# Optimization experiments

Hardware: AMD Instinct MI355X
Metric: run time of the kernel (lower is better)

The kernel has to match this reference:

```python
import jax, jax.numpy as jnp
from jax import lax
import numpy as np

P = 4        # pool_size
NH = 8       # nhead
EPS = 1e-5


def _maxpool(x):
    return lax.reduce_window(x, -jnp.inf, lax.max, (1, 1, P, P), (1, 1, P, P), 'VALID')


def _ln_c(x, g, b):
    # LayerNorm over channel dim of NCHW (torch applies it on NHWC last dim)
    m = x.mean(1, keepdims=True)
    v = x.var(1, keepdims=True)
    return g[None, :, None, None] * (x - m) / jnp.sqrt(v + EPS) + b[None, :, None, None]


def _dwbn(x, w, g, b, rm, rv):
    # depthwise 3x3 conv (groups=C, no bias) + BatchNorm2d (inference, running stats)
    C = x.shape[1]
    y = lax.conv_general_dilated(x, w, (1, 1), ((1, 1), (1, 1)),
                                 dimension_numbers=('NCHW', 'OIHW', 'NCHW'),
                                 feature_group_count=C)
    sc = g / jnp.sqrt(rv + EPS)
    return sc[None, :, None, None] * (y - rm[None, :, None, None]) + b[None, :, None, None]


def _heads(x):
    # n (nhead d) h w -> n (h w) nhead d
    B, C, H, W = x.shape
    return x.reshape(B, NH, C // NH, H * W).transpose(0, 3, 1, 2)


def _fuse(x, m, merge_w, mlp_w1, mlp_w2, ln2_g, ln2_b):
    # merge linear -> reshape to pooled map -> bilinear upsample x4 -> concat -> MLP -> LN -> residual
    B, C, H, W = x.shape
    m = jnp.einsum('nlh d -> nlhd', m) if False else m  # no-op, keep m as [B,L,NH,dim]
    m = m.reshape(B, -1, C) @ merge_w.T                  # [B, L, C]
    m = m.reshape(B, H // P, W // P, C).transpose(0, 3, 1, 2)
    m = jax.image.resize(m, (B, C, H, W), method='bilinear')  # align_corners=False convention
    z = jnp.concatenate([x, m], axis=1).transpose(0, 2, 3, 1)  # NHWC, 2C
    z = jax.nn.relu(z @ mlp_w1.T) @ mlp_w2.T                   # [B,H,W,C]
    mu = z.mean(-1, keepdims=True)
    var = z.var(-1, keepdims=True)
    z = ln2_g * (z - mu) / jnp.sqrt(var + EPS) + ln2_b
    return x + z.transpose(0, 3, 1, 2)


def setup_inputs() -> dict:
    key = jax.random.key(0)
    ks = jax.random.split(key, 20)
    B, C, H, W = 4, 256, 128, 128
    s = 0.05
    return {
        'x1': jax.random.normal(ks[0], (B, C, H, W), jnp.float32),
        'x2': jax.random.normal(ks[1], (B, C, H, W), jnp.float32),
        'qk_w': jax.random.normal(ks[2], (C, 1, 3, 3), jnp.float32) * s,
        'qk_g': 1.0 + 0.1 * jax.random.normal(ks[3], (C,), jnp.float32),
        'qk_b': 0.1 * jax.random.normal(ks[4], (C,), jnp.float32),
        'qk_m': 0.1 * jax.random.normal(ks[5], (C,), jnp.float32),
        'qk_v': jax.random.uniform(ks[6], (C,), jnp.float32, 0.5, 1.5),
        'v_w': jax.random.normal(ks[7], (C, 1, 3, 3), jnp.float32) * s,
        'v_g': 1.0 + 0.1 * jax.random.normal(ks[8], (C,), jnp.float32),
        'v_b': 0.1 * jax.random.normal(ks[9], (C,), jnp.float32),
        'v_m': 0.1 * jax.random.normal(ks[10], (C,), jnp.float32),
        'v_v': jax.random.uniform(ks[11], (C,), jnp.float32, 0.5, 1.5),
        'ln1_g': 1.0 + 0.1 * jax.random.normal(ks[12], (C,), jnp.float32),
        'ln1_b': 0.1 * jax.random.normal(ks[13], (C,), jnp.float32),
        'ln2_g': 1.0 + 0.1 * jax.random.normal(ks[14], (C,), jnp.float32),
        'ln2_b': 0.1 * jax.random.normal(ks[15], (C,), jnp.float32),
        'merge_w': jax.random.normal(ks[16], (C, C), jnp.float32) * s,
        'mlp_w1': jax.random.normal(ks[17], (2 * C, 2 * C), jnp.float32) * s,
        'mlp_w2': jax.random.normal(ks[18], (C, 2 * C), jnp.float32) * s,
    }


def reference(x1, x2, qk_w, qk_g, qk_b, qk_m, qk_v, v_w, v_g, v_b, v_m, v_v,
              ln1_g, ln1_b, ln2_g, ln2_b, merge_w, mlp_w1, mlp_w2):
    # pooled + normalized features (norm1 shared across q/k/v branches)
    p1 = _ln_c(_maxpool(x1), ln1_g, ln1_b)
    p2 = _ln_c(_maxpool(x2), ln1_g, ln1_b)
    query = _heads(_dwbn(p1, qk_w, qk_g, qk_b, qk_m, qk_v))  # [B,L,NH,d]
    key = _heads(_dwbn(p2, qk_w, qk_g, qk_b, qk_m, qk_v))    # [B,S,NH,d]
    v1h = _heads(_dwbn(p1, v_w, v_g, v_b, v_m, v_v))
    v2h = _heads(_dwbn(p2, v_w, v_g, v_b, v_m, v_v))
    QK = jnp.einsum('nlhd,nshd->nlsh', query, key).astype(jnp.float32)
    t = 1.0 / np.sqrt(query.shape[-1]).astype(np.float32)
    S1 = jax.nn.softmax(t * QK, axis=2)   # softmax over s (keys)
    S2 = jax.nn.softmax(t * QK, axis=3)   # softmax over head dim (as in source)
    m1 = jnp.einsum('nlsh,nshd->nlhd', S1, v2h)
    m2 = jnp.einsum('nlsh,nlhd->nshd', S2, v1h)
    out1 = _fuse(x1, m1, merge_w, mlp_w1, mlp_w2, ln2_g, ln2_b)
    out2 = _fuse(x2, m2, merge_w, mlp_w1, mlp_w2, ln2_g, ln2_b)
    return (out1, out2)
```

## Files before the change

### kernel.cpp

```cpp
#include <hip/hip_runtime.h>
#include <hip/hip_bf16.h>

#define NB 4
#define NC 256
#define NH_ 8
#define LPOOL 1024
constexpr float EPSV = 1e-5f;

typedef unsigned short ushort_t;
typedef __attribute__((ext_vector_type(8))) short bf16x8;
typedef __attribute__((ext_vector_type(4))) float f32x4;

#define OFF_P   0u
#define OFF_V2T 1048576u
#define OFF_Q   2097152u
#define OFF_K   3145728u
#define OFF_V1  4194304u
#define OFF_V2  5242880u
#define OFF_M1  6291456u
#define OFF_M2  7340032u
#define OFF_MG  8388608u
#define OFF_A   9437184u
#define OFF_W1B 26214400u
#define OFF_W2B 26345472u
#define OFF_HID 42991616u

__device__ __forceinline__ float bf16_to_f(unsigned short u) {
    union { unsigned int ui; float f; } t; t.ui = ((unsigned int)u) << 16; return t.f;
}
__device__ __forceinline__ unsigned short f_to_bf16(float f) {
    union { float f; unsigned int u; } t; t.f = f;
    unsigned int u = t.u;
    u += 0x7fffu + ((u >> 16) & 1u);
    return (unsigned short)(u >> 16);
}

__global__ __launch_bounds__(256) void pool_kernel(const float* __restrict__ x1,
                                                   const float* __restrict__ x2,
                                                   float* __restrict__ pooled) {
    int idx = blockIdx.x * 256 + threadIdx.x;
    int j = idx & 31, i = (idx >> 5) & 31, c = (idx >> 10) & 255, n = (idx >> 18) & 3, br = idx >> 20;
    const float* xp = br ? x2 : x1;
    const float* base = xp + (((size_t)(n * 256 + c) * 128 + i * 4) * 128 + j * 4);
    float m = -3.4e38f;
#pragma unroll
    for (int r = 0; r < 4; ++r) {
        float4 v = *(const float4*)(base + r * 128);
        m = fmaxf(m, fmaxf(fmaxf(v.x, v.y), fmaxf(v.z, v.w)));
    }
    pooled[(size_t)br * 1048576 + (size_t)(n * 256 + c) * 1024 + i * 32 + j] = m;
}

__global__ __launch_bounds__(256) void lnc_kernel(float* __restrict__ p,
                                                  const float* __restrict__ g,
                                                  const float* __restrict__ b) {
    int bid = blockIdx.x;
    int l = bid & 1023, n = (bid >> 10) & 3, br = bid >> 12;
    int c = threadIdx.x;
    size_t idx = (size_t)br * 1048576 + (size_t)(n * 256 + c) * 1024 + l;
    float v = p[idx];
    __shared__ float red[256];
    red[c] = v; __syncthreads();
    for (int off = 128; off > 0; off >>= 1) { if (c < off) red[c] += red[c + off]; __syncthreads(); }
    float mean = red[0] / 256.f;
    __syncthreads();
    float d = v - mean;
    red[c] = d * d; __syncthreads();
    for (int off = 128; off > 0; off >>= 1) { if (c < off) red[c] += red[c + off]; __syncthreads(); }
    float var = red[0] / 256.f;
    float rstd = rsqrtf(var + EPSV);
    p[idx] = (v - mean) * rstd * g[c] + b[c];
}

__global__ __launch_bounds__(256) void dwbn_kernel(const float* __restrict__ p,
    const float* __restrict__ qkw, const float* __restrict__ qkg, const float* __restrict__ qkb,
    const float* __restrict__ qkm, const float* __restrict__ qkv,
    const float* __restrict__ vw, const float* __restrict__ vg, const float* __restrict__ vb,
    const float* __restrict__ vm, const float* __restrict__ vv,
    float* __restrict__ qkvbuf) {
    int which = blockIdx.y;
    int flat = blockIdx.x * 256 + threadIdx.x;
    int l = flat & 1023, c = (flat >> 10) & 255, n = flat >> 18;
    int br = which & 1;
    const float* w  = (which < 2) ? qkw : vw;
    const float* g  = (which < 2) ? qkg : vg;
    const float* bb = (which < 2) ? qkb : vb;
    const float* rm = (which < 2) ? qkm : vm;
    const float* rv = (which < 2) ? qkv : vv;
    int i = l >> 5, j = l & 31;
    const float* pin = p + (size_t)br * 1048576 + (size_t)(n * 256 + c) * 1024;
    float acc = 0.f;
#pragma unroll
    for (int ky = -1; ky <= 1; ++ky) {
        int yy = i + ky;
        if ((unsigned)yy < 32u) {
#pragma unroll
            for (int kx = -1; kx <= 1; ++kx) {
                int xx = j + kx;
                if ((unsigned)xx < 32u)
                    acc += pin[yy * 32 + xx] * w[c * 9 + (ky + 1) * 3 + (kx + 1)];
            }
        }
    }
    float sc = g[c] * rsqrtf(rv[c] + EPSV);
    qkvbuf[(size_t)which * 1048576 + (size_t)(n * 1024 + l) * 256 + c] = sc * (acc - rm[c]) + bb[c];
}

__global__ __launch_bounds__(256) void cvt_kernel(const float* __restrict__ in,
                                                  ushort_t* __restrict__ out, int n) {
    int i = blockIdx.x * 256 + threadIdx.x;
    if (i < n) out[i] = f_to_bf16(in[i]);
}

__global__ __launch_bounds__(256) void v2t_kernel(const float* __restrict__ v,
                                                  ushort_t* __restrict__ vt) {
    int bid = blockIdx.x;
    int sb = bid & 31, cb = (bid >> 5) & 7, n = bid >> 8;
    int tid = threadIdx.x;
    __shared__ float t[32][33];
    int ci = tid & 31, sg = tid >> 5;
#pragma unroll
    for (int p = 0; p < 4; ++p) {
        int s = sb * 32 + p * 8 + sg;
        t[p * 8 + sg][ci] = v[(size_t)(n * 1024 + s) * 256 + cb * 32 + ci];
    }
    __syncthreads();
    int si = tid & 31, cg = tid >> 5;
#pragma unroll
    for (int p = 0; p < 4; ++p) {
        int c = cb * 32 + p * 8 + cg;
        vt[(size_t)(n * 256 + c) * 1024 + sb * 32 + si] = f_to_bf16(t[si][p * 8 + cg]);
    }
}

__global__ __launch_bounds__(256) void qk_mfma(const ushort_t* __restrict__ qb,
                                               const ushort_t* __restrict__ kb,
                                               float* __restrict__ scores) {
    int lt = blockIdx.x, st = blockIdx.y;
    int nh = blockIdx.z; int n = nh >> 3, h = nh & 7;
    int l0 = lt * 128, s0 = st * 128;
    __shared__ ushort_t Qs[128 * 32];
    __shared__ ushort_t Ks[128 * 32];
    int tid = threadIdx.x, lane = tid & 63, wv = tid >> 6;
    int wm = wv >> 1, wn = wv & 1;
    int ml = lane & 15, quad = lane >> 4;
#pragma unroll
    for (int c = 0; c < 2; ++c) {
        int g = c * 256 + tid;
        int row = g >> 2, seg = g & 3;
        const ushort_t* ga = qb + (size_t)(n * 1024 + l0 + row) * 256 + h * 32 + seg * 8;
        __builtin_amdgcn_global_load_lds((const __attribute__((address_space(1))) void*)ga,
                                         (__attribute__((address_space(3))) void*)&Qs[row * 32 + seg * 8], 16, 0, 0);
        const ushort_t* gk = kb + (size_t)(n * 1024 + s0 + row) * 256 + h * 32 + seg * 8;
        __builtin_amdgcn_global_load_lds((const __attribute__((address_space(1))) void*)gk,
                                         (__attribute__((address_space(3))) void*)&Ks[row * 32 + seg * 8], 16, 0, 0);
    }
    __syncthreads();
    f32x4 acc[4][4];
#pragma unroll
    for (int i = 0; i < 4; ++i)
#pragma unroll
        for (int j = 0; j < 4; ++j) acc[i][j] = (f32x4)(0.f);
    bf16x8 af[4], bfr[4];
#pragma unroll
    for (int mt = 0; mt < 4; ++mt)
        af[mt] = *(const bf16x8*)&Qs[(wm * 64 + mt * 16 + ml) * 32 + quad * 8];
#pragma unroll
    for (int nt = 0; nt < 4; ++nt)
        bfr[nt] = *(const bf16x8*)&Ks[(wn * 64 + nt * 16 + ml) * 32 + quad * 8];
#pragma unroll
    for (int mt = 0; mt < 4; ++mt)
#pragma unroll
        for (int nt = 0; nt < 4; ++nt)
            acc[mt][nt] = __builtin_amdgcn_mfma_f32_16x16x32_bf16(af[mt], bfr[nt], acc[mt][nt], 0, 0, 0);
    const float tsc = 0.17677669529663687f;
    float* sb = scores + (size_t)nh * 1024 * 1024;
#pragma unroll
    for (int mt = 0; mt < 4; ++mt)
#pragma unroll
        for (int nt = 0; nt < 4; ++nt) {
            int col = s0 + wn * 64 + nt * 16 + ml;
#pragma unroll
            for (int r = 0; r < 4; ++r) {
                int row = l0 + wm * 64 + mt * 16 + quad * 4 + r;
                sb[(size_t)row * 1024 + col] = tsc * acc[mt][nt][r];
            }
        }
}

__global__ __launch_bounds__(256) void m1_kernel(const float* __restrict__ scores,
                                                 const ushort_t* __restrict__ v2t,
                                                 float* __restrict__ m1out) {
    int lt = blockIdx.x, h = blockIdx.y, n = blockIdx.z;
    int tid = threadIdx.x, lane = tid & 63, wv = tid >> 6;
    int ml = lane & 15, quad = lane >> 4;
    int l0 = lt * 64 + wv * 16;
    const float* arow = scores + (size_t)((n * 8 + h) * 1024 + l0 + ml) * 1024 + quad * 8;
    const ushort_t* vb = v2t + (size_t)(n * 256 + h * 32) * 1024;
    const ushort_t* vrow0 = vb + (size_t)ml * 1024 + quad * 8;
    const ushort_t* vrow1 = vb + (size_t)(ml + 16) * 1024 + quad * 8;
    f32x4 acc0 = (f32x4)(0.f), acc1 = (f32x4)(0.f);
    float rsum = 0.f;
#pragma unroll 4
    for (int s0 = 0; s0 < 1024; s0 += 32) {
        float4 xa = *(const float4*)(arow + s0);
        float4 xb = *(const float4*)(arow + s0 + 4);
        float e0 = __expf(xa.x), e1 = __expf(xa.y), e2 = __expf(xa.z), e3 = __expf(xa.w);
        float e4 = __expf(xb.x), e5 = __expf(xb.y), e6 = __expf(xb.z), e7 = __expf(xb.w);
        rsum += ((e0 + e1) + (e2 + e3)) + ((e4 + e5) + (e6 + e7));
        bf16x8 af;
        af[0] = (short)f_to_bf16(e0); af[1] = (short)f_to_bf16(e1);
        af[2] = (short)f_to_bf16(e2); af[3] = (short)f_to_bf16(e3);
        af[4] = (short)f_to_bf16(e4); af[5] = (short)f_to_bf16(e5);
        af[6] = (short)f_to_bf16(e6); af[7] = (short)f_to_bf16(e7);
        bf16x8 b0 = *(const bf16x8*)(vrow0 + s0);
        bf16x8 b1 = *(const bf16x8*)(vrow1 + s0);
        acc0 = __builtin_amdgcn_mfma_f32_16x16x32_bf16(af, b0, acc0, 0, 0, 0);
        acc1 = __builtin_amdgcn_mfma_f32_16x16x32_bf16(af, b1, acc1, 0, 0, 0);
    }
    rsum += __shfl_xor(rsum, 16);
    rsum += __shfl_xor(rsum, 32);
#pragma unroll
    for (int r = 0; r < 4; ++r) {
        int row = quad * 4 + r;
        float inv = 1.f / __shfl(rsum, row);
        size_t ob = (size_t)(n * 1024 + l0 + row) * 256 + h * 32;
        m1out[ob + ml] = acc0[r] * inv;
        m1out[ob + 16 + ml] = acc1[r] * inv;
    }
}

__global__ __launch_bounds__(256) void m2_kernel(const float* __restrict__ scores,
                                                 const float* __restrict__ v1,
                                                 float* __restrict__ m2out) {
    int st = blockIdx.x;
    int lc = blockIdx.y;
    int n  = blockIdx.z;
    int s0 = st * 32, tid = threadIdx.x;
    __shared__ float wls[8][8][32];
    float acc[32];
#pragma unroll
    for (int i = 0; i < 32; ++i) acc[i] = 0.f;
    int lA = tid >> 5, siA = tid & 31;
    int hB = tid >> 5;
    const float* sbase = scores + (size_t)n * 8 * 1024 * 1024;
    int lend = lc * 128 + 128;
    for (int lb = lc * 128; lb < lend; lb += 8) {
        int l = lb + lA;
        float e[8];
        float mx = -3.4e38f;
#pragma unroll
        for (int h = 0; h < 8; ++h) {
            e[h] = sbase[((size_t)h * 1024 + l) * 1024 + s0 + siA];
            mx = fmaxf(mx, e[h]);
        }
        float sum = 0.f;
#pragma unroll
        for (int h = 0; h < 8; ++h) { e[h] = expf(e[h] - mx); sum += e[h]; }
        float inv = 1.f / sum;
#pragma unroll
        for (int h = 0; h < 8; ++h) wls[lA][h][siA] = e[h] * inv;
        __syncthreads();
#pragma unroll
        for (int ls = 0; ls < 8; ++ls) {
            float v1v = v1[(size_t)(n * 1024 + lb + ls) * 256 + tid];
#pragma unroll
            for (int s4 = 0; s4 < 8; ++s4) {
                float4 w4 = *(const float4*)&wls[ls][hB][s4 * 4];
                acc[s4 * 4]     += w4.x * v1v;
                acc[s4 * 4 + 1] += w4.y * v1v;
                acc[s4 * 4 + 2] += w4.z * v1v;
                acc[s4 * 4 + 3] += w4.w * v1v;
            }
        }
        __syncthreads();
    }
#pragma unroll
    for (int ss = 0; ss < 32; ++ss)
        atomicAdd(&m2out[(size_t)(n * 1024 + s0 + ss) * 256 + tid], acc[ss]);
}

__global__ __launch_bounds__(256) void merge_kernel(const float* __restrict__ m,
                                                    const float* __restrict__ mw,
                                                    float* __restrict__ merged) {
    int bid = blockIdx.x;
    int n = bid >> 7, lt = bid & 127;
    int l0 = lt * 8, tid = threadIdx.x;
    __shared__ float ms[8][260];
#pragma unroll
    for (int r = 0; r < 8; ++r) ms[r][tid] = m[(size_t)(n * 1024 + l0 + r) * 256 + tid];
    __syncthreads();
    float acc[8];
#pragma unroll
    for (int r = 0; r < 8; ++r) acc[r] = 0.f;
    const float4* wrow = (const float4*)(mw + (size_t)tid * 256);
    for (int c4 = 0; c4 < 64; ++c4) {
        float4 w4 = wrow[c4];
#pragma unroll
        for (int r = 0; r < 8; ++r) {
            float4 m4 = *(const float4*)&ms[r][c4 * 4];
            acc[r] += w4.x * m4.x + w4.y * m4.y + w4.z * m4.z + w4.w * m4.w;
        }
    }
#pragma unroll
    for (int r = 0; r < 8; ++r)
        merged[(size_t)(n * 1024 + l0 + r) * 256 + tid] = acc[r];
}

__global__ __launch_bounds__(256) void zbuild_kernel(const float* __restrict__ x,
                                                     const float* __restrict__ merged,
                                                     ushort_t* __restrict__ z) {
    int pix0 = blockIdx.x * 32;
    int n = pix0 >> 14, y = (pix0 >> 7) & 127, x0 = pix0 & 127;
    int tid = threadIdx.x;
    int ci = tid >> 5, xi = tid & 31;
    __shared__ float xs[256][33];
    for (int cc = 0; cc < 32; ++cc) {
        int c = cc * 8 + ci;
        xs[c][xi] = x[((size_t)(n * 256 + c) * 128 + y) * 128 + x0 + xi];
    }
    __syncthreads();
    float iy = y * 0.25f - 0.375f;
    int y0i = (int)floorf(iy);
    float fy = iy - (float)y0i;
    int y0c = max(y0i, 0), y1c = min(y0i + 1, 31);
    const float* mb = merged + (size_t)n * 1024 * 256;
    for (int xj = 0; xj < 32; ++xj) {
        size_t zb = (size_t)(pix0 + xj) * 512;
        z[zb + tid] = f_to_bf16(xs[tid][xj]);
        int xx = x0 + xj;
        float ix = xx * 0.25f - 0.375f;
        int x0i = (int)floorf(ix);
        float fx = ix - (float)x0i;
        int x0cc = max(x0i, 0), x1cc = min(x0i + 1, 31);
        float v00 = mb[(size_t)(y0c * 32 + x0cc) * 256 + tid];
        float v01 = mb[(size_t)(y0c * 32 + x1cc) * 256 + tid];
        float v10 = mb[(size_t)(y1c * 32 + x0cc) * 256 + tid];
        float v11 = mb[(size_t)(y1c * 32 + x1cc) * 256 + tid];
        float v = (1.f - fy) * ((1.f - fx) * v00 + fx * v01) + fy * ((1.f - fx) * v10 + fx * v11);
        z[zb + 256 + tid] = f_to_bf16(v);
    }
}

__global__ __launch_bounds__(256) void mfma_gemm(const ushort_t* __restrict__ A,
                                                 const ushort_t* __restrict__ B,
                                                 float* __restrict__ Of,
                                                 ushort_t* __restrict__ Oh,
                                                 int N, int relu) {
    const int K = 512;
    int m0 = blockIdx.x * 128, n0 = blockIdx.y * 128;
    int tid = threadIdx.x;
    __shared__ ushort_t Al[128 * 32];
    __shared__ ushort_t Bl[128 * 32];
    int lane = tid & 63;
    int wv = tid >> 6;
    int wm = wv >> 1, wn = wv & 1;
    int ml = lane & 15, quad = lane >> 4;
    f32x4 acc[4][4];
#pragma unroll
    for (int i = 0; i < 4; ++i)
#pragma unroll
        for (int j = 0; j < 4; ++j) acc[i][j] = (f32x4)(0.f);

    for (int k0 = 0; k0 < K; k0 += 32) {
#pragma unroll
        for (int c = 0; c < 2; ++c) {
            int g = c * 256 + tid;
            int row = g >> 2, seg = g & 3;
            const ushort_t* ga = A + (size_t)(m0 + row) * K + k0 + seg * 8;
            __builtin_amdgcn_global_load_lds((const __attribute__((address_space(1))) void*)ga,
                                             (__attribute__((address_space(3))) void*)&Al[g * 8], 16, 0, 0);
            const ushort_t* gb = B + (size_t)(n0 + row) * K + k0 + seg * 8;
            __builtin_amdgcn_global_load_lds((const __attribute__((address_space(1))) void*)gb,
                                             (__attribute__((address_space(3))) void*)&Bl[g * 8], 16, 0, 0);
        }
        __syncthreads();
        bf16x8 af[4], bfr[4];
#pragma unroll
        for (int mt = 0; mt < 4; ++mt)
            af[mt] = *(const bf16x8*)&Al[(wm * 64 + mt * 16 + ml) * 32 + quad * 8];
#pragma unroll
        for (int nt = 0; nt < 4; ++nt)
            bfr[nt] = *(const bf16x8*)&Bl[(wn * 64 + nt * 16 + ml) * 32 + quad * 8];
#pragma unroll
        for (int mt = 0; mt < 4; ++mt)
#pragma unroll
            for (int nt = 0; nt < 4; ++nt)
                acc[mt][nt] = __builtin_amdgcn_mfma_f32_16x16x32_bf16(af[mt], bfr[nt], acc[mt][nt], 0, 0, 0);
        __syncthreads();
    }
#pragma unroll
    for (int mt = 0; mt < 4; ++mt) {
#pragma unroll
        for (int nt = 0; nt < 4; ++nt) {
            int col = n0 + wn * 64 + nt * 16 + ml;
#pragma unroll
            for (int r = 0; r < 4; ++r) {
                int row = m0 + wm * 64 + mt * 16 + quad * 4 + r;
                float v = acc[mt][nt][r];
                if (relu) v = fmaxf(v, 0.f);
                if (Oh) Oh[(size_t)row * N + col] = f_to_bf16(v);
                else    Of[(size_t)row * N + col] = v;
            }
        }
    }
}

__global__ __launch_bounds__(256) void final_kernel(const float* __restrict__ o,
                                                    const float* __restrict__ xin,
                                                    const float* __restrict__ g,
                                                    const float* __restrict__ b,
                                                    float* __restrict__ outp) {
    int xg = blockIdx.x, y = blockIdx.y, n = blockIdx.z;
    int x0 = xg * 32;
    int pix0 = (n * 128 + y) * 128 + x0;
    int tid = threadIdx.x;
    __shared__ float zf[32][257];
    for (int j = 0; j < 32; ++j) zf[j][tid] = o[(size_t)(pix0 + j) * 256 + tid];
    __syncthreads();
    __shared__ float rs[32][9], rq[32][9];
    __shared__ float muA[32], rsA[32];
    int p = tid >> 3, q = tid & 7;
    float s = 0.f, sq = 0.f;
    for (int c = q * 32; c < q * 32 + 32; ++c) { float v = zf[p][c]; s += v; sq += v * v; }
    rs[p][q] = s; rq[p][q] = sq; __syncthreads();
    if (q == 0) {
        float S = 0.f, Q = 0.f;
#pragma unroll
        for (int t = 0; t < 8; ++t) { S += rs[p][t]; Q += rq[p][t]; }
        float mu = S / 256.f;
        float var = Q / 256.f - mu * mu;
        muA[p] = mu; rsA[p] = rsqrtf(var + EPSV);
    }
    __syncthreads();
    int cg = tid >> 5, xi = tid & 31;
    for (int cc = 0; cc < 32; ++cc) {
        int c = cc * 8 + cg;
        float v = (zf[xi][c] - muA[xi]) * rsA[xi] * g[c] + b[c];
        size_t gi = ((size_t)(n * 256 + c) * 128 + y) * 128 + x0 + xi;
        outp[gi] = xin[gi] + v;
    }
}

extern "C" void kernel_launch(void* const* d_in, const int* in_sizes, int n_in,
                              void* d_out, int out_size, void* d_ws, size_t ws_size,
                              hipStream_t stream) {
    (void)in_sizes; (void)n_in; (void)out_size; (void)ws_size;
    const float* x1     = (const float*)d_in[0];
    const float* x2     = (const float*)d_in[1];
    const float* qk_w   = (const float*)d_in[2];
    const float* qk_g   = (const float*)d_in[3];
    const float* qk_b   = (const float*)d_in[4];
    const float* qk_m   = (const float*)d_in[5];
    const float* qk_v   = (const float*)d_in[6];
    const float* v_w    = (const float*)d_in[7];
    const float* v_g    = (const float*)d_in[8];
    const float* v_b    = (const float*)d_in[9];
    const float* v_m    = (const float*)d_in[10];
    const float* v_v    = (const float*)d_in[11];
    const float* ln1_g  = (const float*)d_in[12];
    const float* ln1_b  = (const float*)d_in[13];
    const float* ln2_g  = (const float*)d_in[14];
    const float* ln2_b  = (const float*)d_in[15];
    const float* merge_w = (const float*)d_in[16];
    const float* mlp_w1 = (const float*)d_in[17];
    const float* mlp_w2 = (const float*)d_in[18];

    float* ws      = (float*)d_ws;
    float* pooled  = ws + OFF_P;
    float* qkvbuf  = ws + OFF_Q;
    float* v1buf   = ws + OFF_V1;
    float* v2buf   = ws + OFF_V2;
    float* m1buf   = ws + OFF_M1;
    float* m2buf   = ws + OFF_M2;
    float* mgbuf   = ws + OFF_MG;
    float* regA    = ws + OFF_A;
    ushort_t* qkb16 = (ushort_t*)(ws + OFF_P);
    ushort_t* v2tb = (ushort_t*)(ws + OFF_V2T);
    ushort_t* zb16 = (ushort_t*)(ws + OFF_A);
    ushort_t* w1b  = (ushort_t*)(ws + OFF_W1B);
    ushort_t* w2b  = (ushort_t*)(ws + OFF_W2B);
    ushort_t* hid  = (ushort_t*)(ws + OFF_HID);
    float* outp    = (float*)d_out;

    hipMemsetAsync(m2buf, 0, 1048576 * sizeof(float), stream);

    pool_kernel<<<8192, 256, 0, stream>>>(x1, x2, pooled);
    lnc_kernel<<<8192, 256, 0, stream>>>(pooled, ln1_g, ln1_b);
    dwbn_kernel<<<dim3(4096, 4), 256, 0, stream>>>(pooled,
        qk_w, qk_g, qk_b, qk_m, qk_v, v_w, v_g, v_b, v_m, v_v, qkvbuf);
    cvt_kernel<<<8192, 256, 0, stream>>>(qkvbuf, qkb16, 2097152);
    v2t_kernel<<<1024, 256, 0, stream>>>(v2buf, v2tb);
    qk_mfma<<<dim3(8, 8, 32), 256, 0, stream>>>(qkb16, qkb16 + 1048576, regA);
    m1_kernel<<<dim3(16, 8, 4), 256, 0, stream>>>(regA, v2tb, m1buf);
    m2_kernel<<<dim3(32, 8, 4), 256, 0, stream>>>(regA, v1buf, m2buf);

    cvt_kernel<<<1024, 256, 0, stream>>>(mlp_w1, w1b, 262144);
    cvt_kernel<<<512, 256, 0, stream>>>(mlp_w2, w2b, 131072);

    for (int br = 0; br < 2; ++br) {
        const float* xin = br ? x2 : x1;
        const float* mm  = br ? m2buf : m1buf;
        merge_kernel<<<512, 256, 0, stream>>>(mm, merge_w, mgbuf);
        zbuild_kernel<<<2048, 256, 0, stream>>>(xin, mgbuf, zb16);
        mfma_gemm<<<dim3(512, 4), 256, 0, stream>>>(zb16, w1b, nullptr, hid, 512, 1);
        mfma_gemm<<<dim3(512, 2), 256, 0, stream>>>(hid, w2b, regA, nullptr, 256, 0);
        final_kernel<<<dim3(4, 128, 4), 256, 0, stream>>>(regA, xin, ln2_g, ln2_b,
                                                          outp + (size_t)br * 16777216);
    }
}
```

Measured before the change: 816.1 us.

## Fuse MLP GEMMs with LayerNorm/residual and store attention scores in bf16

Replaces the two separate MLP GEMM launches and the final LayerNorm/residual kernel with a single fused kernel per branch. Each block computes a 64-row tile of the hidden layer, keeps it in swizzled LDS, and then runs the second GEMM, the LayerNorm and the residual add before writing NCHW output. This removes the global round trips for the hidden activations and the pre-norm output. Attention scores are also written and read as bf16 instead of fp32, which halves score traffic but lowers softmax input precision. The fused kernel reads A/B operands straight from global memory without LDS staging and uses a large LDS footprint, which may limit occupancy.

```diff
diff --git a/kernel.cpp b/kernel.cpp
--- a/kernel.cpp
+++ b/kernel.cpp
@@ -23,7 +23,6 @@
 #define OFF_A   9437184u
 #define OFF_W1B 26214400u
 #define OFF_W2B 26345472u
-#define OFF_HID 42991616u
 
 __device__ __forceinline__ float bf16_to_f(unsigned short u) {
     union { unsigned int ui; float f; } t; t.ui = ((unsigned int)u) << 16; return t.f;
@@ -135,7 +134,7 @@
 
 __global__ __launch_bounds__(256) void qk_mfma(const ushort_t* __restrict__ qb,
                                                const ushort_t* __restrict__ kb,
-                                               float* __restrict__ scores) {
+                                               ushort_t* __restrict__ scores) {
     int lt = blockIdx.x, st = blockIdx.y;
     int nh = blockIdx.z; int n = nh >> 3, h = nh & 7;
     int l0 = lt * 128, s0 = st * 128;
@@ -174,7 +173,7 @@
         for (int nt = 0; nt < 4; ++nt)
             acc[mt][nt] = __builtin_amdgcn_mfma_f32_16x16x32_bf16(af[mt], bfr[nt], acc[mt][nt], 0, 0, 0);
     const float tsc = 0.17677669529663687f;
-    float* sb = scores + (size_t)nh * 1024 * 1024;
+    ushort_t* sb = scores + (size_t)nh * 1024 * 1024;
 #pragma unroll
     for (int mt = 0; mt < 4; ++mt)
 #pragma unroll
@@ -183,19 +182,24 @@
 #pragma unroll
             for (int r = 0; r < 4; ++r) {
                 int row = l0 + wm * 64 + mt * 16 + quad * 4 + r;
-                sb[(size_t)row * 1024 + col] = tsc * acc[mt][nt][r];
+                unsigned short b = f_to_bf16(tsc * acc[mt][nt][r]);
+                int partner = __shfl_xor((int)b, 1);
+                if (!(ml & 1)) {
+                    unsigned int pk = (unsigned int)b | ((unsigned int)partner << 16);
+                    *(unsigned int*)&sb[(size_t)row * 1024 + col] = pk;
+                }
             }
         }
 }
 
-__global__ __launch_bounds__(256) void m1_kernel(const float* __restrict__ scores,
+__global__ __launch_bounds__(256) void m1_kernel(const ushort_t* __restrict__ scores,
                                                  const ushort_t* __restrict__ v2t,
                                                  float* __restrict__ m1out) {
     int lt = blockIdx.x, h = blockIdx.y, n = blockIdx.z;
     int tid = threadIdx.x, lane = tid & 63, wv = tid >> 6;
     int ml = lane & 15, quad = lane >> 4;
     int l0 = lt * 64 + wv * 16;
-    const float* arow = scores + (size_t)((n * 8 + h) * 1024 + l0 + ml) * 1024 + quad * 8;
+    const ushort_t* arow = scores + (size_t)((n * 8 + h) * 1024 + l0 + ml) * 1024 + quad * 8;
     const ushort_t* vb = v2t + (size_t)(n * 256 + h * 32) * 1024;
     const ushort_t* vrow0 = vb + (size_t)ml * 1024 + quad * 8;
     const ushort_t* vrow1 = vb + (size_t)(ml + 16) * 1024 + quad * 8;
@@ -203,10 +207,15 @@
     float rsum = 0.f;
 #pragma unroll 4
     for (int s0 = 0; s0 < 1024; s0 += 32) {
-        float4 xa = *(const float4*)(arow + s0);
-        float4 xb = *(const float4*)(arow + s0 + 4);
-        float e0 = __expf(xa.x), e1 = __expf(xa.y), e2 = __expf(xa.z), e3 = __expf(xa.w);
-        float e4 = __expf(xb.x), e5 = __expf(xb.y), e6 = __expf(xb.z), e7 = __expf(xb.w);
+        bf16x8 sv = *(const bf16x8*)(arow + s0);
+        float e0 = __expf(bf16_to_f((ushort_t)sv[0]));
+        float e1 = __expf(bf16_to_f((ushort_t)sv[1]));
+        float e2 = __expf(bf16_to_f((ushort_t)sv[2]));
+        float e3 = __expf(bf16_to_f((ushort_t)sv[3]));
+        float e4 = __expf(bf16_to_f((ushort_t)sv[4]));
+        float e5 = __expf(bf16_to_f((ushort_t)sv[5]));
+        float e6 = __expf(bf16_to_f((ushort_t)sv[6]));
+        float e7 = __expf(bf16_to_f((ushort_t)sv[7]));
         rsum += ((e0 + e1) + (e2 + e3)) + ((e4 + e5) + (e6 + e7));
         bf16x8 af;
         af[0] = (short)f_to_bf16(e0); af[1] = (short)f_to_bf16(e1);
@@ -230,7 +239,7 @@
     }
 }
 
-__global__ __launch_bounds__(256) void m2_kernel(const float* __restrict__ scores,
+__global__ __launch_bounds__(256) void m2_kernel(const ushort_t* __restrict__ scores,
                                                  const float* __restrict__ v1,
                                                  float* __restrict__ m2out) {
     int st = blockIdx.x;
@@ -243,7 +252,7 @@
     for (int i = 0; i < 32; ++i) acc[i] = 0.f;
     int lA = tid >> 5, siA = tid & 31;
     int hB = tid >> 5;
-    const float* sbase = scores + (size_t)n * 8 * 1024 * 1024;
+    const ushort_t* sbase = scores + (size_t)n * 8 * 1024 * 1024;
     int lend = lc * 128 + 128;
     for (int lb = lc * 128; lb < lend; lb += 8) {
         int l = lb + lA;
@@ -251,7 +260,7 @@
         float mx = -3.4e38f;
 #pragma unroll
         for (int h = 0; h < 8; ++h) {
-            e[h] = sbase[((size_t)h * 1024 + l) * 1024 + s0 + siA];
+            e[h] = bf16_to_f(sbase[((size_t)h * 1024 + l) * 1024 + s0 + siA]);
             mx = fmaxf(mx, e[h]);
         }
         float sum = 0.f;
@@ -342,103 +351,134 @@
     }
 }
 
-__global__ __launch_bounds__(256) void mfma_gemm(const ushort_t* __restrict__ A,
-                                                 const ushort_t* __restrict__ B,
-                                                 float* __restrict__ Of,
-                                                 ushort_t* __restrict__ Oh,
-                                                 int N, int relu) {
-    const int K = 512;
-    int m0 = blockIdx.x * 128, n0 = blockIdx.y * 128;
-    int tid = threadIdx.x;
-    __shared__ ushort_t Al[128 * 32];
-    __shared__ ushort_t Bl[128 * 32];
-    int lane = tid & 63;
-    int wv = tid >> 6;
+__global__ __launch_bounds__(256) void mlp_fused(const ushort_t* __restrict__ Z,
+                                                 const ushort_t* __restrict__ W1,
+                                                 const ushort_t* __restrict__ W2,
+                                                 const float* __restrict__ xin,
+                                                 const float* __restrict__ g2,
+                                                 const float* __restrict__ b2,
+                                                 float* __restrict__ outp) {
+    __shared__ char smem[67584];
+    float* olds = (float*)smem;
+    float* redS = (float*)(smem + 65792);
+    float* redQ = (float*)(smem + 66304);
+    float* muA  = (float*)(smem + 66816);
+    float* rsA  = (float*)(smem + 67072);
+
+    int m0 = blockIdx.x * 64;
+    int tid = threadIdx.x, lane = tid & 63, wv = tid >> 6;
+    int ml = lane & 15, quad = lane >> 4;
+
+    {
+        f32x4 acc[4][8];
+#pragma unroll
+        for (int i = 0; i < 4; ++i)
+#pragma unroll
+            for (int j = 0; j < 8; ++j) acc[i][j] = (f32x4)(0.f);
+#pragma unroll 2
+        for (int k0 = 0; k0 < 512; k0 += 32) {
+            bf16x8 af[4], bfr[8];
+#pragma unroll
+            for (int mt = 0; mt < 4; ++mt)
+                af[mt] = *(const bf16x8*)&Z[(size_t)(m0 + mt * 16 + ml) * 512 + k0 + quad * 8];
+#pragma unroll
+            for (int nt = 0; nt < 8; ++nt)
+                bfr[nt] = *(const bf16x8*)&W1[(size_t)(wv * 128 + nt * 16 + ml) * 512 + k0 + quad * 8];
+#pragma unroll
+            for (int mt = 0; mt < 4; ++mt)
+#pragma unroll
+                for (int nt = 0; nt < 8; ++nt)
+                    acc[mt][nt] = __builtin_amdgcn_mfma_f32_16x16x32_bf16(af[mt], bfr[nt], acc[mt][nt], 0, 0, 0);
+        }
+#pragma unroll
+        for (int mt = 0; mt < 4; ++mt)
+#pragma unroll
+            for (int nt = 0; nt < 8; ++nt)
+#pragma unroll
+                for (int r = 0; r < 4; ++r) {
+                    int row = mt * 16 + quad * 4 + r;
+                    int col = wv * 128 + nt * 16 + ml;
+                    unsigned byte = ((unsigned)(row * 512 + col) * 2u) ^ ((unsigned)(row & 7) << 4);
+                    *(ushort_t*)(smem + byte) = f_to_bf16(fmaxf(acc[mt][nt][r], 0.f));
+                }
+    }
+    __syncthreads();
     int wm = wv >> 1, wn = wv & 1;
-    int ml = lane & 15, quad = lane >> 4;
-    f32x4 acc[4][4];
-#pragma unroll
-    for (int i = 0; i < 4; ++i)
-#pragma unroll
-        for (int j = 0; j < 4; ++j) acc[i][j] = (f32x4)(0.f);
-
-    for (int k0 = 0; k0 < K; k0 += 32) {
-#pragma unroll
-        for (int c = 0; c < 2; ++c) {
-            int g = c * 256 + tid;
-            int row = g >> 2, seg = g & 3;
-            const ushort_t* ga = A + (size_t)(m0 + row) * K + k0 + seg * 8;
-            __builtin_amdgcn_global_load_lds((const __attribute__((address_space(1))) void*)ga,
-                                             (__attribute__((address_space(3))) void*)&Al[g * 8], 16, 0, 0);
-            const ushort_t* gb = B + (size_t)(n0 + row) * K + k0 + seg * 8;
-            __builtin_amdgcn_global_load_lds((const __attribute__((address_space(1))) void*)gb,
-                                             (__attribute__((address_space(3))) void*)&Bl[g * 8], 16, 0, 0);
-        }
-        __syncthreads();
-        bf16x8 af[4], bfr[4];
-#pragma unroll
-        for (int mt = 0; mt < 4; ++mt)
-            af[mt] = *(const bf16x8*)&Al[(wm * 64 + mt * 16 + ml) * 32 + quad * 8];
-#pragma unroll
-        for (int nt = 0; nt < 4; ++nt)
-            bfr[nt] = *(const bf16x8*)&Bl[(wn * 64 + nt * 16 + ml) * 32 + quad * 8];
-#pragma unroll
-        for (int mt = 0; mt < 4; ++mt)
-#pragma unroll
-            for (int nt = 0; nt < 4; ++nt)
-                acc[mt][nt] = __builtin_amdgcn_mfma_f32_16x16x32_bf16(af[mt], bfr[nt], acc[mt][nt], 0, 0, 0);
-        __syncthreads();
-    }
-#pragma unroll
-    for (int mt = 0; mt < 4; ++mt) {
-#pragma unroll
-        for (int nt = 0; nt < 4; ++nt) {
-            int col = n0 + wn * 64 + nt * 16 + ml;
-#pragma unroll
-            for (int r = 0; r < 4; ++r) {
-                int row = m0 + wm * 64 + mt * 16 + quad * 4 + r;
-                float v = acc[mt][nt][r];
-                if (relu) v = fmaxf(v, 0.f);
-                if (Oh) Oh[(size_t)row * N + col] = f_to_bf16(v);
-                else    Of[(size_t)row * N + col] = v;
+    f32x4 a2[2][8];
+#pragma unroll
+    for (int i = 0; i < 2; ++i)
+#pragma unroll
+        for (int j = 0; j < 8; ++j) a2[i][j] = (f32x4)(0.f);
+#pragma unroll 2
+    for (int k0 = 0; k0 < 512; k0 += 32) {
+        bf16x8 af2[2], bf2[8];
+#pragma unroll
+        for (int mt = 0; mt < 2; ++mt) {
+            int row = wm * 32 + mt * 16 + ml;
+            unsigned byte = ((unsigned)(row * 1024 + k0 * 2 + quad * 16)) ^ ((unsigned)(row & 7) << 4);
+            af2[mt] = *(const bf16x8*)(smem + byte);
+        }
+#pragma unroll
+        for (int nt = 0; nt < 8; ++nt)
+            bf2[nt] = *(const bf16x8*)&W2[(size_t)(wn * 128 + nt * 16 + ml) * 512 + k0 + quad * 8];
+#pragma unroll
+        for (int mt = 0; mt < 2; ++mt)
+#pragma unroll
+            for (int nt = 0; nt < 8; ++nt)
+                a2[mt][nt] = __builtin_amdgcn_mfma_f32_16x16x32_bf16(af2[mt], bf2[nt], a2[mt][nt], 0, 0, 0);
+    }
+#pragma unroll
+    for (int mt = 0; mt < 2; ++mt)
+#pragma unroll
+        for (int r = 0; r < 4; ++r) {
+            float s = 0.f, q = 0.f;
+#pragma unroll
+            for (int nt = 0; nt < 8; ++nt) { float v = a2[mt][nt][r]; s += v; q += v * v; }
+            s += __shfl_xor(s, 1); s += __shfl_xor(s, 2); s += __shfl_xor(s, 4); s += __shfl_xor(s, 8);
+            q += __shfl_xor(q, 1); q += __shfl_xor(q, 2); q += __shfl_xor(q, 4); q += __shfl_xor(q, 8);
+            if (ml == 0) {
+                int row = wm * 32 + mt * 16 + quad * 4 + r;
+                redS[row * 2 + wn] = s; redQ[row * 2 + wn] = q;
             }
         }
-    }
-}
-
-__global__ __launch_bounds__(256) void final_kernel(const float* __restrict__ o,
-                                                    const float* __restrict__ xin,
-                                                    const float* __restrict__ g,
-                                                    const float* __restrict__ b,
-                                                    float* __restrict__ outp) {
-    int xg = blockIdx.x, y = blockIdx.y, n = blockIdx.z;
-    int x0 = xg * 32;
-    int pix0 = (n * 128 + y) * 128 + x0;
-    int tid = threadIdx.x;
-    __shared__ float zf[32][257];
-    for (int j = 0; j < 32; ++j) zf[j][tid] = o[(size_t)(pix0 + j) * 256 + tid];
-    __syncthreads();
-    __shared__ float rs[32][9], rq[32][9];
-    __shared__ float muA[32], rsA[32];
-    int p = tid >> 3, q = tid & 7;
-    float s = 0.f, sq = 0.f;
-    for (int c = q * 32; c < q * 32 + 32; ++c) { float v = zf[p][c]; s += v; sq += v * v; }
-    rs[p][q] = s; rq[p][q] = sq; __syncthreads();
-    if (q == 0) {
-        float S = 0.f, Q = 0.f;
-#pragma unroll
-        for (int t = 0; t < 8; ++t) { S += rs[p][t]; Q += rq[p][t]; }
-        float mu = S / 256.f;
-        float var = Q / 256.f - mu * mu;
-        muA[p] = mu; rsA[p] = rsqrtf(var + EPSV);
-    }
-    __syncthreads();
+    __syncthreads();
+    if (tid < 64) {
+        float S = redS[tid * 2] + redS[tid * 2 + 1];
+        float Q = redQ[tid * 2] + redQ[tid * 2 + 1];
+        float mu = S * (1.f / 256.f);
+        float var = Q * (1.f / 256.f) - mu * mu;
+        muA[tid] = mu; rsA[tid] = rsqrtf(var + EPSV);
+    }
+    __syncthreads();
+    float gv[8], bv[8];
+#pragma unroll
+    for (int nt = 0; nt < 8; ++nt) {
+        int col = wn * 128 + nt * 16 + ml;
+        gv[nt] = g2[col]; bv[nt] = b2[col];
+    }
+#pragma unroll
+    for (int mt = 0; mt < 2; ++mt)
+#pragma unroll
+        for (int r = 0; r < 4; ++r) {
+            int row = wm * 32 + mt * 16 + quad * 4 + r;
+            float mu = muA[row], rs = rsA[row];
+#pragma unroll
+            for (int nt = 0; nt < 8; ++nt) {
+                int col = wn * 128 + nt * 16 + ml;
+                olds[row * 257 + col] = (a2[mt][nt][r] - mu) * rs * gv[nt] + bv[nt];
+            }
+        }
+    __syncthreads();
+    int n = m0 >> 14, y = (m0 >> 7) & 127, x0 = m0 & 127;
     int cg = tid >> 5, xi = tid & 31;
     for (int cc = 0; cc < 32; ++cc) {
         int c = cc * 8 + cg;
-        float v = (zf[xi][c] - muA[xi]) * rsA[xi] * g[c] + b[c];
-        size_t gi = ((size_t)(n * 256 + c) * 128 + y) * 128 + x0 + xi;
-        outp[gi] = xin[gi] + v;
+        size_t gbase = ((size_t)(n * 256 + c) * 128 + y) * 128 + x0;
+#pragma unroll
+        for (int xc = 0; xc < 2; ++xc) {
+            int p = xc * 32 + xi;
+            outp[gbase + p] = xin[gbase + p] + olds[p * 257 + c];
+        }
     }
 }
 
@@ -474,13 +514,12 @@
     float* m1buf   = ws + OFF_M1;
     float* m2buf   = ws + OFF_M2;
     float* mgbuf   = ws + OFF_MG;
-    float* regA    = ws + OFF_A;
+    ushort_t* scores16 = (ushort_t*)(ws + OFF_A);
     ushort_t* qkb16 = (ushort_t*)(ws + OFF_P);
     ushort_t* v2tb = (ushort_t*)(ws + OFF_V2T);
     ushort_t* zb16 = (ushort_t*)(ws + OFF_A);
     ushort_t* w1b  = (ushort_t*)(ws + OFF_W1B);
     ushort_t* w2b  = (ushort_t*)(ws + OFF_W2B);
-    ushort_t* hid  = (ushort_t*)(ws + OFF_HID);
     float* outp    = (float*)d_out;
 
     hipMemsetAsync(m2buf, 0, 1048576 * sizeof(float), stream);
@@ -491,9 +530,9 @@
         qk_w, qk_g, qk_b, qk_m, qk_v, v_w, v_g, v_b, v_m, v_v, qkvbuf);
     cvt_kernel<<<8192, 256, 0, stream>>>(qkvbuf, qkb16, 2097152);
     v2t_kernel<<<1024, 256, 0, stream>>>(v2buf, v2tb);
-    qk_mfma<<<dim3(8, 8, 32), 256, 0, stream>>>(qkb16, qkb16 + 1048576, regA);
-    m1_kernel<<<dim3(16, 8, 4), 256, 0, stream>>>(regA, v2tb, m1buf);
-    m2_kernel<<<dim3(32, 8, 4), 256, 0, stream>>>(regA, v1buf, m2buf);
+    qk_mfma<<<dim3(8, 8, 32), 256, 0, stream>>>(qkb16, qkb16 + 1048576, scores16);
+    m1_kernel<<<dim3(16, 8, 4), 256, 0, stream>>>(scores16, v2tb, m1buf);
+    m2_kernel<<<dim3(32, 8, 4), 256, 0, stream>>>(scores16, v1buf, m2buf);
 
     cvt_kernel<<<1024, 256, 0, stream>>>(mlp_w1, w1b, 262144);
     cvt_kernel<<<512, 256, 0, stream>>>(mlp_w2, w2b, 131072);
@@ -503,9 +542,7 @@
         const float* mm  = br ? m2buf : m1buf;
         merge_kernel<<<512, 256, 0, stream>>>(mm, merge_w, mgbuf);
         zbuild_kernel<<<2048, 256, 0, stream>>>(xin, mgbuf, zb16);
-        mfma_gemm<<<dim3(512, 4), 256, 0, stream>>>(zb16, w1b, nullptr, hid, 512, 1);
-        mfma_gemm<<<dim3(512, 2), 256, 0, stream>>>(hid, w2b, regA, nullptr, 256, 0);
-        final_kernel<<<dim3(4, 128, 4), 256, 0, stream>>>(regA, xin, ln2_g, ln2_b,
-                                                          outp + (size_t)br * 16777216);
-    }
-}
+        mlp_fused<<<1024, 256, 0, stream>>>(zb16, w1b, w2b, xin, ln2_g, ln2_b,
+                                            outp + (size_t)br * 16777216);
+    }
+}
```

Result: slower. 922.9 us (+13.1%).
